# Kernel tuning notes

Hardware: AMD Instinct MI355X
Metric: run time of the kernel (lower is better)

Reference implementation:

```python
import jax, jax.numpy as jnp
import numpy as np

VAR0, VAR1 = 0.1, 0.2          # SSD encode variances
POS_T, NEG_T, NPR = 0.5, 0.4, 3  # pos/neg thresholds, negpos_ratio
BBOX_ALPHA, CONF_ALPHA = 1.5, 1.0


def point_form(b):
    # cxcywh -> x1y1x2y2
    return jnp.concatenate([b[..., :2] - b[..., 2:] / 2, b[..., :2] + b[..., 2:] / 2], -1)


def jaccard(a, b):
    # a:[n,4], b:[m,4] in xyxy -> IoU [n,m]
    tl = jnp.maximum(a[:, None, :2], b[None, :, :2])
    br = jnp.minimum(a[:, None, 2:], b[None, :, 2:])
    inter = jnp.prod(jnp.clip(br - tl, 0.0), -1)
    area_a = jnp.prod(a[:, 2:] - a[:, :2], -1)[:, None]
    area_b = jnp.prod(b[:, 2:] - b[:, :2], -1)[None, :]
    return inter / jnp.clip(area_a + area_b - inter, 1e-10)


def encode(matched, priors):
    # matched: xyxy GT per prior; priors: cxcywh
    g_c = ((matched[:, :2] + matched[:, 2:]) / 2 - priors[:, :2]) / (VAR0 * priors[:, 2:])
    g_wh = jnp.log(jnp.clip((matched[:, 2:] - matched[:, :2]) / priors[:, 2:], 1e-8)) / VAR1
    return jnp.concatenate([g_c, g_wh], -1)


def match_one(gt_box, gt_lab, priors):
    # gt_box:[G,4] xyxy, gt_lab:[G], priors:[P,4] cxcywh
    ov = jaccard(gt_box, point_form(priors))            # [G,P]
    bt_over = ov.max(0)                                  # best GT overlap per prior [P]
    bt_idx = ov.argmax(0)                                # [P]
    bp_idx = ov.argmax(1)                                # best prior per GT [G]
    G = gt_box.shape[0]
    bt_over = bt_over.at[bp_idx].set(2.0)                # force-match best priors
    bt_idx = bt_idx.at[bp_idx].set(jnp.arange(G))
    matched = gt_box[bt_idx]                             # [P,4]
    conf_t = gt_lab[bt_idx]
    conf_t = jnp.where(bt_over < POS_T, jnp.where(bt_over < NEG_T, 0, -1), conf_t)
    return encode(matched, priors), conf_t


def reference(loc_data, conf_data, priors, gt_bboxes, gt_labels):
    B, P, C = conf_data.shape
    loc_t, conf_t = jax.vmap(match_one)(gt_bboxes, gt_labels, priors)
    loc_t = jax.lax.stop_gradient(loc_t)                 # targets are detached in torch
    pos = conf_t > 0                                     # [B,P]
    num_pos = pos.sum(-1)                                # [B]
    dt = loc_data.dtype
    pos_w = pos.astype(dt) / jnp.clip(num_pos, 1).astype(dt)[:, None]

    # localization: per-image-normalized smooth L1 over positives
    d = loc_data - loc_t
    sl1 = jnp.where(jnp.abs(d) < 1.0, 0.5 * d * d, jnp.abs(d) - 0.5)
    loss_B = (pos_w[:, :, None] * sl1).sum() * BBOX_ALPHA

    # OHEM confidence loss: mine top negpos_ratio*num_pos hardest negatives per image
    loss_c = jax.nn.logsumexp(conf_data, -1) - conf_data[..., 0]
    loss_c = jnp.where(pos | (conf_t < 0), 0.0, jax.lax.stop_gradient(loss_c))
    rank = jnp.argsort(jnp.argsort(-loss_c, -1), -1)     # descending rank [B,P]
    num_neg = jnp.clip(NPR * num_pos, 0, P - 1)
    neg = (rank < num_neg[:, None]) & (conf_t == 0)
    keep = (pos | neg).astype(dt)
    logp = jax.nn.log_softmax(conf_data, -1)
    tgt = jnp.clip(conf_t, 0)
    ce = -jnp.take_along_axis(logp, tgt[..., None], -1)[..., 0]
    loss_C = (keep * ce).sum() * CONF_ALPHA

    return jnp.stack([loss_B, loss_C]) / B               # [2]: (loss_B, loss_C)


def setup_inputs() -> dict:
    key = jax.random.key(0)
    k = jax.random.split(key, 8)
    B, P, C, G = 16, 19248, 81, 16
    loc_data = jax.random.normal(k[0], (B, P, 4), jnp.float32)
    conf_data = jax.random.normal(k[1], (B, P, C), jnp.float32)
    pc = jax.random.uniform(k[2], (B, P, 2)) * 0.9 + 0.05
    pwh = jax.random.uniform(k[3], (B, P, 2)) * 0.25 + 0.05
    priors = jnp.concatenate([pc, pwh], -1).astype(jnp.float32)  # cxcywh
    gc = jax.random.uniform(k[4], (B, G, 2)) * 0.8 + 0.1
    gwh = jax.random.uniform(k[5], (B, G, 2)) * 0.3 + 0.05
    gt_bboxes = jnp.clip(point_form(jnp.concatenate([gc, gwh], -1)), 0.0, 1.0).astype(jnp.float32)
    gt_labels = jax.random.randint(k[6], (B, G), 1, C)
    return {"loc_data": loc_data, "conf_data": conf_data, "priors": priors,
            "gt_bboxes": gt_bboxes, "gt_labels": gt_labels}
```

## Files before the change

kernel.cpp:

```cpp
#include <hip/hip_runtime.h>
#include <math.h>

#define NB 16
#define NP 19248
#define NC 81
#define NG 16
#define NBLK 76

static __device__ __forceinline__ float smoothl1(float d) {
    float a = fabsf(d);
    return (a < 1.f) ? 0.5f * d * d : (a - 0.5f);
}

static __device__ __forceinline__ unsigned long long umax64(unsigned long long a, unsigned long long b) {
    return a > b ? a : b;
}

__global__ void k_init(unsigned int* w, float* out) {
    if (threadIdx.x < 512) w[threadIdx.x] = 0u;
    if (threadIdx.x < 2) out[threadIdx.x] = 0.f;
}

__global__ void k_match(const float* __restrict__ priors,
                        const float* __restrict__ gtb,
                        float* __restrict__ bt_over, int* __restrict__ bt_idx,
                        unsigned long long* __restrict__ bp_key) {
    const int b = blockIdx.y;
    const int p = blockIdx.x * 256 + threadIdx.x;
    const bool valid = p < NP;
    __shared__ float4 sgt[NG];
    __shared__ unsigned long long smax[NG];
    if (threadIdx.x < NG) {
        const float* g4 = gtb + (size_t)(b * NG + threadIdx.x) * 4;
        sgt[threadIdx.x] = make_float4(g4[0], g4[1], g4[2], g4[3]);
        smax[threadIdx.x] = 0ULL;
    }
    __syncthreads();
    float4 pr = make_float4(0.f, 0.f, 0.f, 0.f);
    if (valid) pr = *(const float4*)(priors + ((size_t)b * NP + p) * 4);
    float px1 = pr.x - pr.z * 0.5f, py1 = pr.y - pr.w * 0.5f;
    float px2 = pr.x + pr.z * 0.5f, py2 = pr.y + pr.w * 0.5f;
    float areaP = (px2 - px1) * (py2 - py1);
    float best = -1.f; int bi = 0;
    unsigned int pk = 0xFFFFFFFFu - (unsigned int)p;
    #pragma unroll
    for (int g = 0; g < NG; ++g) {
        float4 gb = sgt[g];
        float iw = fminf(gb.z, px2) - fmaxf(gb.x, px1);
        float ih = fminf(gb.w, py2) - fmaxf(gb.y, py1);
        float inter = fmaxf(iw, 0.f) * fmaxf(ih, 0.f);
        float areaG = (gb.z - gb.x) * (gb.w - gb.y);
        float ov = inter / fmaxf(areaG + areaP - inter, 1e-10f);
        if (ov > best) { best = ov; bi = g; }
        unsigned long long key = ((unsigned long long)__float_as_uint(ov) << 32) | pk;
        #pragma unroll
        for (int off = 32; off >= 1; off >>= 1)
            key = umax64(key, (unsigned long long)__shfl_xor((unsigned long long)key, off));
        if ((threadIdx.x & 63) == 0) atomicMax(&smax[g], key);
    }
    if (valid) {
        bt_over[(size_t)b * NP + p] = best;
        bt_idx[(size_t)b * NP + p] = bi;
    }
    __syncthreads();
    if (threadIdx.x < NG) atomicMax(&bp_key[b * NG + threadIdx.x], smax[threadIdx.x]);
}

__global__ void __launch_bounds__(256, 3) k_conf(
        const float* __restrict__ conf,
        const float* __restrict__ loc,
        const float* __restrict__ priors,
        const float* __restrict__ gtb,
        const int* __restrict__ gtl,
        const float* __restrict__ bt_over,
        const int* __restrict__ bt_idx,
        const unsigned long long* __restrict__ bp_key,
        int* __restrict__ conf_t_a,
        float* __restrict__ mlc,
        float* __restrict__ ce,
        int* __restrict__ pnp, float* __restrict__ psl, float* __restrict__ pce) {
    const int b = blockIdx.y;
    const int p = blockIdx.x * 256 + threadIdx.x;
    const bool valid = p < NP;
    const int pc = valid ? p : (NP - 1);
    const int bp = b * NP + pc;

    const long long p81 = (long long)bp * 81;
    const int off = (int)(p81 & 3);
    const float4* q = (const float4*)(conf + (p81 - off));
    float4 r[21];
    #pragma unroll
    for (int i = 0; i < 21; ++i) r[i] = q[i];

    const float over = bt_over[bp];
    int bi = bt_idx[bp];
    int ct;
    if (over < 0.4f) ct = 0;
    else if (over < 0.5f) ct = -1;
    else ct = gtl[b * NG + bi];
    #pragma unroll
    for (int g = NG - 1; g >= 0; --g) {
        unsigned int fp = 0xFFFFFFFFu - (unsigned int)(bp_key[b * NG + g] & 0xFFFFFFFFULL);
        if (fp == (unsigned int)p) { bi = g; ct = gtl[b * NG + g]; break; }
    }
    if (!valid) ct = 0;
    const int tgt = ct > 0 ? ct : 0;

    float s0 = 0.f, s1 = 0.f, s2 = 0.f, s3 = 0.f;
    #pragma unroll
    for (int i = 0; i < 21; ++i) {
        float4 v = r[i];
        if (i == 0) {
            if (off <= 0) s0 += __expf(v.x);
            if (off <= 1) s1 += __expf(v.y);
            if (off <= 2) s2 += __expf(v.z);
            s3 += __expf(v.w);
        } else if (i == 20) {
            s0 += __expf(v.x);
            if (off >= 1) s1 += __expf(v.y);
            if (off >= 2) s2 += __expf(v.z);
            if (off >= 3) s3 += __expf(v.w);
        } else {
            s0 += __expf(v.x); s1 += __expf(v.y);
            s2 += __expf(v.z); s3 += __expf(v.w);
        }
    }
    const float s = (s0 + s1) + (s2 + s3);
    const float c0 = (off == 0) ? r[0].x : (off == 1) ? r[0].y : (off == 2) ? r[0].z : r[0].w;
    const float ctg = (tgt == 0) ? c0 : conf[p81 + tgt];
    const float lse = __logf(s);
    const float cev = lse - ctg;

    if (valid) {
        ce[bp] = cev;
        conf_t_a[bp] = ct;
        mlc[bp] = (ct == 0) ? (lse - c0) : 0.f;
    }
    float vsl = 0.f, vce = 0.f; int vnp = 0;
    if (ct > 0) {
        const float4 pr = *(const float4*)(priors + (size_t)bp * 4);
        const float* gb = gtb + (size_t)(b * NG + bi) * 4;
        float lt0 = ((gb[0] + gb[2]) * 0.5f - pr.x) / (0.1f * pr.z);
        float lt1 = ((gb[1] + gb[3]) * 0.5f - pr.y) / (0.1f * pr.w);
        float lt2 = logf(fmaxf((gb[2] - gb[0]) / pr.z, 1e-8f)) / 0.2f;
        float lt3 = logf(fmaxf((gb[3] - gb[1]) / pr.w, 1e-8f)) / 0.2f;
        const float4 l4 = *(const float4*)(loc + (size_t)bp * 4);
        vsl = smoothl1(l4.x - lt0) + smoothl1(l4.y - lt1) +
              smoothl1(l4.z - lt2) + smoothl1(l4.w - lt3);
        vce = cev;
        vnp = 1;
    }
    #pragma unroll
    for (int o = 32; o >= 1; o >>= 1) {
        vnp += __shfl_xor(vnp, o);
        vsl += __shfl_xor(vsl, o);
        vce += __shfl_xor(vce, o);
    }
    __shared__ int snp[4]; __shared__ float ssl[4], sce2[4];
    const int w = threadIdx.x >> 6;
    if ((threadIdx.x & 63) == 0) { snp[w] = vnp; ssl[w] = vsl; sce2[w] = vce; }
    __syncthreads();
    if (threadIdx.x == 0) {
        const int idx = b * NBLK + blockIdx.x;
        pnp[idx] = snp[0] + snp[1] + snp[2] + snp[3];
        psl[idx] = ssl[0] + ssl[1] + ssl[2] + ssl[3];
        pce[idx] = sce2[0] + sce2[1] + sce2[2] + sce2[3];
    }
}

__global__ void __launch_bounds__(1024) k_selneg(
        const float* __restrict__ mlc,
        const int* __restrict__ conf_t_a,
        const float* __restrict__ ce,
        const int* __restrict__ pnp,
        const float* __restrict__ psl,
        const float* __restrict__ pce,
        float* __restrict__ out) {
    const int b = blockIdx.x, tid = threadIdx.x;
    __shared__ unsigned int hist[4096];
    __shared__ unsigned long long list[1024];
    __shared__ unsigned int s_jstar, s_need, s_cnt;
    __shared__ unsigned long long s_thr;
    __shared__ unsigned int wtot[16], wsuf[16];
    __shared__ float wsum[16];
    __shared__ int s_np; __shared__ float s_sl, s_cp;

    if (tid < 64) {
        int np_ = 0; float sl_ = 0.f, cp_ = 0.f;
        for (int i = tid; i < NBLK; i += 64) {
            np_ += pnp[b * NBLK + i];
            sl_ += psl[b * NBLK + i];
            cp_ += pce[b * NBLK + i];
        }
        #pragma unroll
        for (int o = 32; o >= 1; o >>= 1) {
            np_ += __shfl_xor(np_, o);
            sl_ += __shfl_xor(sl_, o);
            cp_ += __shfl_xor(cp_, o);
        }
        if (tid == 0) { s_np = np_; s_sl = sl_; s_cp = cp_; }
    }
    if (tid == 0) { s_cnt = 0u; s_thr = ~0ULL; }
    __syncthreads();
    const int np = s_np;
    const unsigned int k = (unsigned int)min(3 * np, NP - 1);
    const float* vals = mlc + (size_t)b * NP;

    if (k > 0) {
        for (int i = tid; i < 4096; i += 1024) hist[i] = 0u;
        __syncthreads();
        for (int p = tid; p < NP; p += 1024)
            atomicAdd(&hist[min((unsigned int)(vals[p] * 256.f), 4095u)], 1u);
        __syncthreads();
        unsigned int c0 = hist[tid * 4], c1 = hist[tid * 4 + 1],
                     c2 = hist[tid * 4 + 2], c3 = hist[tid * 4 + 3];
        unsigned int t2 = c2 + c3, t1 = c1 + t2, t0 = c0 + t1;
        unsigned int s = t0;
        const int lane = tid & 63, w = tid >> 6;
        #pragma unroll
        for (int o = 1; o < 64; o <<= 1) {
            unsigned int vv = __shfl_down(s, o);
            if (lane + o < 64) s += vv;
        }
        if (lane == 0) wtot[w] = s;
        __syncthreads();
        if (tid < 16) {
            unsigned int acc = 0;
            for (int j = tid + 1; j < 16; ++j) acc += wtot[j];
            wsuf[tid] = acc;
        }
        __syncthreads();
        const unsigned int base = wsuf[w] + (s - t0);
        unsigned int b0 = base + t0, b1 = base + t1, b2 = base + t2, b3 = base + c3;
        hist[tid * 4] = b0; hist[tid * 4 + 1] = b1;
        hist[tid * 4 + 2] = b2; hist[tid * 4 + 3] = b3;
        __syncthreads();
        unsigned int n3 = (tid * 4 + 4 < 4096) ? hist[tid * 4 + 4] : 0u;
        if (b0 >= k && b1 < k) { s_jstar = tid * 4;     s_need = k - b1; }
        if (b1 >= k && b2 < k) { s_jstar = tid * 4 + 1; s_need = k - b2; }
        if (b2 >= k && b3 < k) { s_jstar = tid * 4 + 2; s_need = k - b3; }
        if (b3 >= k && n3 < k) { s_jstar = tid * 4 + 3; s_need = k - n3; }
        __syncthreads();
        const unsigned int jstar = s_jstar, need = s_need;
        for (int p = tid; p < NP; p += 1024) {
            float v = vals[p];
            if (min((unsigned int)(v * 256.f), 4095u) == jstar) {
                unsigned int pos = atomicAdd(&s_cnt, 1u);
                if (pos < 1024u)
                    list[pos] = ((unsigned long long)__float_as_uint(v) << 32) |
                                (unsigned long long)(0xFFFFFFFFu - (unsigned int)p);
            }
        }
        __syncthreads();
        const unsigned int cnt = s_cnt;
        if (cnt <= 1024u) {
            if (tid < (int)cnt) {
                unsigned long long me = list[tid];
                unsigned int rk = 0;
                for (unsigned int j = 0; j < cnt; ++j) rk += (list[j] > me) ? 1u : 0u;
                if (rk == need - 1) s_thr = me;
            }
        } else if (tid == 0) {
            s_thr = ((unsigned long long)__float_as_uint((float)jstar / 256.f)) << 32;
        }
    }
    __syncthreads();
    const unsigned long long thr = s_thr;

    float sum = 0.f;
    const int* cta = conf_t_a + (size_t)b * NP;
    const float* ceb = ce + (size_t)b * NP;
    for (int p = tid; p < NP; p += 1024) {
        if (cta[p] == 0) {
            unsigned long long key = ((unsigned long long)__float_as_uint(vals[p]) << 32) |
                                     (unsigned long long)(0xFFFFFFFFu - (unsigned int)p);
            if (key >= thr) sum += ceb[p];
        }
    }
    #pragma unroll
    for (int o = 32; o >= 1; o >>= 1) sum += __shfl_xor(sum, o);
    if ((tid & 63) == 0) wsum[tid >> 6] = sum;
    __syncthreads();
    if (tid == 0) {
        float neg = 0.f;
        #pragma unroll
        for (int i = 0; i < 16; ++i) neg += wsum[i];
        float lb = s_sl / (float)max(np, 1);
        float lc = s_cp + neg;
        atomicAdd(&out[0], lb * 1.5f / (float)NB);
        atomicAdd(&out[1], lc / (float)NB);
    }
}

extern "C" void kernel_launch(void* const* d_in, const int* in_sizes, int n_in,
                              void* d_out, int out_size, void* d_ws, size_t ws_size,
                              hipStream_t stream) {
    const float* loc    = (const float*)d_in[0];
    const float* conf   = (const float*)d_in[1];
    const float* priors = (const float*)d_in[2];
    const float* gtb    = (const float*)d_in[3];
    const int*   gtl    = (const int*)d_in[4];
    float* out = (float*)d_out;

    char* w = (char*)d_ws;
    const size_t BP4 = (size_t)NB * NP * 4;
    unsigned long long* bp_key = (unsigned long long*)w;
    int*   pnp = (int*)  (w + 4096);
    float* psl = (float*)(w + 4096 + NB * NBLK * 4);
    float* pce = (float*)(w + 4096 + 2 * NB * NBLK * 4);
    float* bt_over  = (float*)(w + 32768);
    int*   bt_idx   = (int*)  (w + 32768 + BP4);
    int*   conf_t_a = (int*)  (w + 32768 + 2 * BP4);
    float* mlc      = (float*)(w + 32768 + 3 * BP4);
    float* ce       = (float*)(w + 32768 + 4 * BP4);

    k_init<<<1, 512, 0, stream>>>((unsigned int*)w, out);
    k_match<<<dim3(NBLK, NB), 256, 0, stream>>>(priors, gtb, bt_over, bt_idx, bp_key);
    k_conf<<<dim3(NBLK, NB), 256, 0, stream>>>(conf, loc, priors, gtb, gtl,
                                               bt_over, bt_idx, bp_key, conf_t_a, mlc, ce,
                                               pnp, psl, pce);
    k_selneg<<<NB, 1024, 0, stream>>>(mlc, conf_t_a, ce, pnp, psl, pce, out);
}
```

Before: 208.9 us.

## Drop ce/conf_t buffers, encode negatives in mlc sentinel, vectorize selection scans

For negatives the CE value equals the mining loss (lse - c0), so k_conf now writes only mlc, with -1 marking non-negative priors. The separate ce and conf_t arrays and their reads in k_selneg go away. k_selneg uses float4 loads for its three passes and skips the threshold search when k covers all negatives. Launch bounds occupancy goes from 3 to 4 blocks, which may raise register pressure for the 21-float4 row buffer.

```diff
diff --git a/kernel.cpp b/kernel.cpp
--- a/kernel.cpp
+++ b/kernel.cpp
@@ -66,7 +66,7 @@
     if (threadIdx.x < NG) atomicMax(&bp_key[b * NG + threadIdx.x], smax[threadIdx.x]);
 }
 
-__global__ void __launch_bounds__(256, 3) k_conf(
+__global__ void __launch_bounds__(256, 4) k_conf(
         const float* __restrict__ conf,
         const float* __restrict__ loc,
         const float* __restrict__ priors,
@@ -75,9 +75,7 @@
         const float* __restrict__ bt_over,
         const int* __restrict__ bt_idx,
         const unsigned long long* __restrict__ bp_key,
-        int* __restrict__ conf_t_a,
         float* __restrict__ mlc,
-        float* __restrict__ ce,
         int* __restrict__ pnp, float* __restrict__ psl, float* __restrict__ pce) {
     const int b = blockIdx.y;
     const int p = blockIdx.x * 256 + threadIdx.x;
@@ -127,17 +125,13 @@
     }
     const float s = (s0 + s1) + (s2 + s3);
     const float c0 = (off == 0) ? r[0].x : (off == 1) ? r[0].y : (off == 2) ? r[0].z : r[0].w;
-    const float ctg = (tgt == 0) ? c0 : conf[p81 + tgt];
     const float lse = __logf(s);
-    const float cev = lse - ctg;
-
-    if (valid) {
-        ce[bp] = cev;
-        conf_t_a[bp] = ct;
-        mlc[bp] = (ct == 0) ? (lse - c0) : 0.f;
-    }
+
+    if (valid) mlc[bp] = (ct == 0) ? (lse - c0) : -1.0f;
+
     float vsl = 0.f, vce = 0.f; int vnp = 0;
     if (ct > 0) {
+        const float ctg = conf[p81 + tgt];
         const float4 pr = *(const float4*)(priors + (size_t)bp * 4);
         const float* gb = gtb + (size_t)(b * NG + bi) * 4;
         float lt0 = ((gb[0] + gb[2]) * 0.5f - pr.x) / (0.1f * pr.z);
@@ -147,7 +141,7 @@
         const float4 l4 = *(const float4*)(loc + (size_t)bp * 4);
         vsl = smoothl1(l4.x - lt0) + smoothl1(l4.y - lt1) +
               smoothl1(l4.z - lt2) + smoothl1(l4.w - lt3);
-        vce = cev;
+        vce = lse - ctg;
         vnp = 1;
     }
     #pragma unroll
@@ -170,8 +164,6 @@
 
 __global__ void __launch_bounds__(1024) k_selneg(
         const float* __restrict__ mlc,
-        const int* __restrict__ conf_t_a,
-        const float* __restrict__ ce,
         const int* __restrict__ pnp,
         const float* __restrict__ psl,
         const float* __restrict__ pce,
@@ -204,13 +196,18 @@
     __syncthreads();
     const int np = s_np;
     const unsigned int k = (unsigned int)min(3 * np, NP - 1);
-    const float* vals = mlc + (size_t)b * NP;
+    const float4* v4 = (const float4*)(mlc + (size_t)b * NP);
 
     if (k > 0) {
         for (int i = tid; i < 4096; i += 1024) hist[i] = 0u;
         __syncthreads();
-        for (int p = tid; p < NP; p += 1024)
-            atomicAdd(&hist[min((unsigned int)(vals[p] * 256.f), 4095u)], 1u);
+        for (int i = tid; i < NP / 4; i += 1024) {
+            float4 v = v4[i];
+            if (v.x >= 0.f) atomicAdd(&hist[min((unsigned int)(v.x * 256.f), 4095u)], 1u);
+            if (v.y >= 0.f) atomicAdd(&hist[min((unsigned int)(v.y * 256.f), 4095u)], 1u);
+            if (v.z >= 0.f) atomicAdd(&hist[min((unsigned int)(v.z * 256.f), 4095u)], 1u);
+            if (v.w >= 0.f) atomicAdd(&hist[min((unsigned int)(v.w * 256.f), 4095u)], 1u);
+        }
         __syncthreads();
         unsigned int c0 = hist[tid * 4], c1 = hist[tid * 4 + 1],
                      c2 = hist[tid * 4 + 2], c3 = hist[tid * 4 + 3];
@@ -235,46 +232,59 @@
         hist[tid * 4] = b0; hist[tid * 4 + 1] = b1;
         hist[tid * 4 + 2] = b2; hist[tid * 4 + 3] = b3;
         __syncthreads();
-        unsigned int n3 = (tid * 4 + 4 < 4096) ? hist[tid * 4 + 4] : 0u;
-        if (b0 >= k && b1 < k) { s_jstar = tid * 4;     s_need = k - b1; }
-        if (b1 >= k && b2 < k) { s_jstar = tid * 4 + 1; s_need = k - b2; }
-        if (b2 >= k && b3 < k) { s_jstar = tid * 4 + 2; s_need = k - b3; }
-        if (b3 >= k && n3 < k) { s_jstar = tid * 4 + 3; s_need = k - n3; }
-        __syncthreads();
-        const unsigned int jstar = s_jstar, need = s_need;
-        for (int p = tid; p < NP; p += 1024) {
-            float v = vals[p];
-            if (min((unsigned int)(v * 256.f), 4095u) == jstar) {
-                unsigned int pos = atomicAdd(&s_cnt, 1u);
-                if (pos < 1024u)
-                    list[pos] = ((unsigned long long)__float_as_uint(v) << 32) |
-                                (unsigned long long)(0xFFFFFFFFu - (unsigned int)p);
+        const unsigned int total = hist[0];
+        if (k >= total) {
+            if (tid == 0) s_thr = 0ULL;
+        } else {
+            unsigned int n3 = (tid * 4 + 4 < 4096) ? hist[tid * 4 + 4] : 0u;
+            if (b0 >= k && b1 < k) { s_jstar = tid * 4;     s_need = k - b1; }
+            if (b1 >= k && b2 < k) { s_jstar = tid * 4 + 1; s_need = k - b2; }
+            if (b2 >= k && b3 < k) { s_jstar = tid * 4 + 2; s_need = k - b3; }
+            if (b3 >= k && n3 < k) { s_jstar = tid * 4 + 3; s_need = k - n3; }
+            __syncthreads();
+            const unsigned int jstar = s_jstar, need = s_need;
+            for (int i = tid; i < NP / 4; i += 1024) {
+                float4 v = v4[i];
+                float vv[4] = {v.x, v.y, v.z, v.w};
+                #pragma unroll
+                for (int c = 0; c < 4; ++c) {
+                    if (vv[c] >= 0.f &&
+                        min((unsigned int)(vv[c] * 256.f), 4095u) == jstar) {
+                        unsigned int pos = atomicAdd(&s_cnt, 1u);
+                        if (pos < 1024u)
+                            list[pos] = ((unsigned long long)__float_as_uint(vv[c]) << 32) |
+                                        (unsigned long long)(0xFFFFFFFFu - (unsigned int)(4 * i + c));
+                    }
+                }
             }
-        }
-        __syncthreads();
-        const unsigned int cnt = s_cnt;
-        if (cnt <= 1024u) {
-            if (tid < (int)cnt) {
-                unsigned long long me = list[tid];
-                unsigned int rk = 0;
-                for (unsigned int j = 0; j < cnt; ++j) rk += (list[j] > me) ? 1u : 0u;
-                if (rk == need - 1) s_thr = me;
+            __syncthreads();
+            const unsigned int cnt = s_cnt;
+            if (cnt <= 1024u) {
+                if (tid < (int)cnt) {
+                    unsigned long long me = list[tid];
+                    unsigned int rk = 0;
+                    for (unsigned int j = 0; j < cnt; ++j) rk += (list[j] > me) ? 1u : 0u;
+                    if (rk == need - 1) s_thr = me;
+                }
+            } else if (tid == 0) {
+                s_thr = ((unsigned long long)__float_as_uint((float)jstar / 256.f)) << 32;
             }
-        } else if (tid == 0) {
-            s_thr = ((unsigned long long)__float_as_uint((float)jstar / 256.f)) << 32;
         }
     }
     __syncthreads();
     const unsigned long long thr = s_thr;
 
     float sum = 0.f;
-    const int* cta = conf_t_a + (size_t)b * NP;
-    const float* ceb = ce + (size_t)b * NP;
-    for (int p = tid; p < NP; p += 1024) {
-        if (cta[p] == 0) {
-            unsigned long long key = ((unsigned long long)__float_as_uint(vals[p]) << 32) |
-                                     (unsigned long long)(0xFFFFFFFFu - (unsigned int)p);
-            if (key >= thr) sum += ceb[p];
+    for (int i = tid; i < NP / 4; i += 1024) {
+        float4 v = v4[i];
+        float vv[4] = {v.x, v.y, v.z, v.w};
+        #pragma unroll
+        for (int c = 0; c < 4; ++c) {
+            if (vv[c] >= 0.f) {
+                unsigned long long key = ((unsigned long long)__float_as_uint(vv[c]) << 32) |
+                                         (unsigned long long)(0xFFFFFFFFu - (unsigned int)(4 * i + c));
+                if (key >= thr) sum += vv[c];
+            }
         }
     }
     #pragma unroll
@@ -310,14 +320,12 @@
     float* pce = (float*)(w + 4096 + 2 * NB * NBLK * 4);
     float* bt_over  = (float*)(w + 32768);
     int*   bt_idx   = (int*)  (w + 32768 + BP4);
-    int*   conf_t_a = (int*)  (w + 32768 + 2 * BP4);
-    float* mlc      = (float*)(w + 32768 + 3 * BP4);
-    float* ce       = (float*)(w + 32768 + 4 * BP4);
+    float* mlc      = (float*)(w + 32768 + 2 * BP4);
 
     k_init<<<1, 512, 0, stream>>>((unsigned int*)w, out);
     k_match<<<dim3(NBLK, NB), 256, 0, stream>>>(priors, gtb, bt_over, bt_idx, bp_key);
     k_conf<<<dim3(NBLK, NB), 256, 0, stream>>>(conf, loc, priors, gtb, gtl,
-                                               bt_over, bt_idx, bp_key, conf_t_a, mlc, ce,
+                                               bt_over, bt_idx, bp_key, mlc,
                                                pnp, psl, pce);
-    k_selneg<<<NB, 1024, 0, stream>>>(mlc, conf_t_a, ce, pnp, psl, pce, out);
-}
+    k_selneg<<<NB, 1024, 0, stream>>>(mlc, pnp, psl, pce, out);
+}
```

Measured after the change: 189.4 us. -9.3%, faster.
